# Kernel optimization log

Measured on AMD Instinct MI355X. Metric: run time of the kernel, lower is better.

## Reference

```python
import jax, jax.numpy as jnp
import numpy as np
from jax import lax

B, C_IN, N, K = 4, 128, 4096, 16
C_OUT = 256
EPS = 1e-5


def setup_inputs() -> dict:
    key = jax.random.key(0)
    k1, k2, k3, k4, k5 = jax.random.split(key, 5)
    x = jax.random.normal(k1, (B, C_IN, N, 1), dtype=jnp.float32)
    y = jax.random.normal(k2, (B, C_IN, N, 1), dtype=jnp.float32)
    edge_index = jax.random.randint(k3, (2, B, N, K), 0, N)
    # Conv2d(in=2*C_IN, out=C_OUT, kernel 3x3), kaiming-ish scale
    fan_in = 2 * C_IN * 9
    conv_w = jax.random.normal(k4, (C_OUT, 2 * C_IN, 3, 3), dtype=jnp.float32) * (2.0 / fan_in) ** 0.5
    conv_b = jnp.zeros((C_OUT,), dtype=jnp.float32)
    gamma = jnp.ones((C_OUT,), dtype=jnp.float32)
    beta = jnp.zeros((C_OUT,), dtype=jnp.float32)
    _ = k5
    return {"x": x, "y": y, "edge_index": edge_index,
            "conv_w": conv_w, "conv_b": conv_b, "gamma": gamma, "beta": beta}


def _batched_index_select(feat, idx):
    # feat: [B, C, N, 1], idx: [B, N, K] -> [B, C, N, K]
    fs = feat[..., 0]  # [B, C, N]
    return jax.vmap(lambda fb, ib: fb[:, ib])(fs, idx)


def reference(x, y, edge_index, conv_w, conv_b, gamma, beta):
    x_i = _batched_index_select(x, edge_index[1])        # [B, C, N, K]
    x_j = _batched_index_select(y, edge_index[0])        # [B, C, N, K]
    h = jnp.concatenate([x_i, x_j - x_i], axis=1)        # [B, 2C, N, K]
    out = lax.conv_general_dilated(
        h, conv_w, window_strides=(1, 1), padding=((1, 1), (1, 1)),
        dimension_numbers=("NCHW", "OIHW", "NCHW"))
    out = out + conv_b[None, :, None, None]
    # BatchNorm2d in training mode: biased batch statistics per channel
    mean = jnp.mean(out, axis=(0, 2, 3), keepdims=True)
    var = jnp.mean((out - mean) ** 2, axis=(0, 2, 3), keepdims=True)
    out = gamma[None, :, None, None] * (out - mean) * lax.rsqrt(var + EPS) + beta[None, :, None, None]
    out = jax.nn.relu(out)
    return jnp.max(out, axis=-1, keepdims=True)          # [B, C_OUT, N, 1]
```

## Files before the change

kernel.cpp:

```cpp
#include <hip/hip_runtime.h>

typedef unsigned short u16;
typedef unsigned int u32;
typedef __attribute__((ext_vector_type(8))) u16 u16x8;
typedef __attribute__((ext_vector_type(8))) __bf16 bf16x8;
typedef __attribute__((ext_vector_type(4))) float f32x4;

#define CIN 128
#define NB 4
#define NN 4096
#define KPTS 16
#define COUT 256
#define POSB 65536
#define TOTPOS 262144
#define CK 2304

__device__ __forceinline__ float bf2f(u16 u){ return __uint_as_float(((u32)u)<<16); }
__device__ __forceinline__ u16 f2bf(float f){
  u32 u = __float_as_uint(f);
  u32 r = (u + 0x7fffu + ((u>>16)&1u)) >> 16;
  return (u16)r;
}

__global__ void pack_w_kernel(const float* __restrict__ w, u16* __restrict__ wp){
  int t = blockIdx.x*256 + threadIdx.x;
  if (t >= COUT*CK) return;
  int co = t / CK; int r = t - co*CK; int tap = r >> 8; int c = r & 255;
  float v;
  if (c < 128)
    v = w[(co*256 + c)*9 + tap] - w[(co*256 + 128 + c)*9 + tap];
  else
    v = w[(co*256 + c)*9 + tap];
  wp[t] = f2bf(v);
}

__global__ void transpose_cast_kernel(const float* __restrict__ x, const float* __restrict__ y,
                                      u16* __restrict__ xt, u16* __restrict__ yt){
  __shared__ u16 tile[2][32][65];
  int n0 = blockIdx.x*64, c0 = blockIdx.y*32, b = blockIdx.z;
  int t = threadIdx.x;
  int tn = t & 63, tc = t >> 6;
  #pragma unroll
  for (int i=0;i<8;++i){
    int c = tc*8 + i;
    size_t src = ((size_t)(b*CIN + c0 + c))*NN + n0 + tn;
    tile[0][c][tn] = f2bf(x[src]);
    tile[1][c][tn] = f2bf(y[src]);
  }
  __syncthreads();
  int tcc = t & 31, tnn = t >> 5;
  #pragma unroll
  for (int i=0;i<8;++i){
    int n = tnn*8 + i;
    size_t dst = ((size_t)(b*NN + n0 + n))*CIN + c0 + tcc;
    xt[dst] = tile[0][tcc][n];
    yt[dst] = tile[1][tcc][n];
  }
}

#define SWZ(row, chunk) (((row)*32) + ((((chunk) ^ (((row)>>1)&3))) << 3))

__global__ __launch_bounds__(256) void conv_gemm_kernel(const u16* __restrict__ wp,
    const int* __restrict__ e, const u16* __restrict__ xt, const u16* __restrict__ yt,
    const u16* __restrict__ zrow, const float* __restrict__ bias,
    float* __restrict__ ssum, float* __restrict__ ssq, float* __restrict__ maxout){
  __shared__ u16 als[3*4096];
  __shared__ u16 pnl[2*6144];

  int bid = blockIdx.x;
  int co_half = (bid >> 3) & 1;
  int ptile = (bid & 7) | ((bid >> 4) << 3);
  int p0 = ptile * 128;
  int b = p0 >> 16;
  int pib0 = p0 & (POSB-1);
  int nb0 = pib0 >> 4;

  int t = threadIdx.x;
  int lane = t & 63, wave = t >> 6;
  int wr = wave >> 1, wc = wave & 1;
  int co_base = co_half*128;
  int l15 = lane & 15, l4 = lane >> 4;

  const u16* xb = xt + ((size_t)b)*NN*CIN;
  const u16* yb = yt + ((size_t)b)*NN*CIN;

  int r0 = wave*32 + (lane>>2);
  int r1 = r0 + 16;
  int ch0 = (lane&3) ^ ((r0>>1)&3);
  int ch1 = (lane&3) ^ ((r1>>1)&3);
  int wuni = __builtin_amdgcn_readfirstlane(wave);
  int wu  = wuni*1024;
  int wu2 = wuni*512;
  const u16* pA0 = wp + (size_t)(co_base + r0)*CK + ch0*8;
  const u16* pA1 = wp + (size_t)(co_base + r1)*CK + ch1*8;

  const u16 *xp[3], *yp[3];
  { int tq4 = t >> 2;
    #pragma unroll
    for (int i=0;i<3;++i){
      int row = i*64 + tq4;
      int lc = (t&3) ^ ((row>>1)&3);
      int q = (row*57) >> 10;
      int kk = row - q*18 - 1;
      int n2 = nb0 - 1 + q;
      bool valid = (row < 180) && ((unsigned)n2 < (unsigned)NN) && ((unsigned)kk < (unsigned)KPTS);
      int j0 = 0, j1 = 0;
      if (valid){ int eo = b*POSB + n2*16 + kk; j0 = e[eo]; j1 = e[TOTPOS + eo]; }
      xp[i] = (valid ? xb + (size_t)j1*CIN : zrow) + lc*8;
      yp[i] = (valid ? yb + (size_t)j0*CIN : zrow) + lc*8;
    }
  }

  auto G16 = [&](const u16* g, u16* l){
    __builtin_amdgcn_global_load_lds((const __attribute__((address_space(1))) u32*)g,
                                     (__attribute__((address_space(3))) u32*)l, 16, 0, 0);
  };

  f32x4 acc[4][4];
  #pragma unroll
  for (int i=0;i<4;++i)
    #pragma unroll
    for (int j=0;j<4;++j) acc[i][j] = (f32x4){0.f,0.f,0.f,0.f};

  G16(xp[0],    &pnl[wu2]);
  G16(xp[1],    &pnl[2048+wu2]);
  G16(xp[2],    &pnl[4096+wu2]);
  G16(xp[0]+32, &pnl[6144+wu2]);
  G16(xp[1]+32, &pnl[6144+2048+wu2]);
  G16(xp[2]+32, &pnl[6144+4096+wu2]);
  G16(pA0,      &als[wu]);      G16(pA1,      &als[wu+512]);
  G16(pA0+256,  &als[4096+wu]); G16(pA1+256,  &als[4096+wu+512]);
  G16(pA0+512,  &als[8192+wu]); G16(pA1+512,  &als[8192+wu+512]);

  int aoff[4];
  #pragma unroll
  for (int f=0; f<4; ++f) aoff[f] = SWZ(wr*64 + f*16 + l15, l4);
  int wc72l15 = wc*72 + l15;

  bf16x8 f0_a[4], f0_b[4], f1_a[4], f1_b[4];

  asm volatile("s_waitcnt vmcnt(4)" ::: "memory");
  __builtin_amdgcn_s_barrier();
  #pragma unroll
  for (int f=0; f<4; ++f) f0_a[f] = *(bf16x8*)&als[aoff[f]];
  #pragma unroll
  for (int f=0; f<4; ++f){
    int r = wc72l15 + f*18;
    f0_b[f] = *(bf16x8*)&pnl[r*32 + ((l4 ^ ((r>>1)&3))<<3)];
  }

  #define STEP(TAU, CUR, NXT) { \
    asm volatile("s_waitcnt lgkmcnt(0)" ::: "memory"); \
    __builtin_amdgcn_s_barrier(); \
    { int chs = (c + (((TAU)>=6)?1:0)) & 7; \
      int koff = ((((TAU)+3)%9)*256) + (chs<<5); \
      G16(pA0 + koff, &als[(((TAU)%3)*4096) + wu]); \
      G16(pA1 + koff, &als[(((TAU)%3)*4096) + wu + 512]); } \
    if ((TAU)==0){ int cc=(c+1)&7; int co32=(cc&3)*32; \
      const u16* s0=(cc<4?xp[0]:yp[0])+co32; \
      const u16* s1=(cc<4?xp[1]:yp[1])+co32; \
      const u16* s2=(cc<4?xp[2]:yp[2])+co32; \
      int pd=((c+1)&1)*6144; \
      G16(s0,&pnl[pd+wu2]); G16(s1,&pnl[pd+2048+wu2]); G16(s2,&pnl[pd+4096+wu2]); } \
    if ((TAU)<=1) asm volatile("s_waitcnt vmcnt(7)" ::: "memory"); \
    else          asm volatile("s_waitcnt vmcnt(4)" ::: "memory"); \
    __builtin_amdgcn_s_barrier(); \
    if ((c < 7) || ((TAU) < 8)){ \
      _Pragma("unroll") \
      for (int f=0; f<4; ++f) NXT##_a[f] = *(bf16x8*)&als[((((TAU)+1)%3)*4096) + aoff[f]]; \
      const u16* pb = ((TAU)==8) ? pbN : pbC; \
      const int tq = ((TAU)+1)%9; \
      const int kbc = (tq/3)*18 + (tq%3); \
      _Pragma("unroll") \
      for (int f=0; f<4; ++f){ int r = wc72l15 + kbc + f*18; \
        NXT##_b[f] = *(bf16x8*)&pb[r*32 + ((l4 ^ ((r>>1)&3))<<3)]; } \
    } \
    __builtin_amdgcn_sched_barrier(0); \
    __builtin_amdgcn_s_setprio(1); \
    _Pragma("unroll") \
    for (int fm=0; fm<4; ++fm) \
      _Pragma("unroll") \
      for (int fn=0; fn<4; ++fn) \
        acc[fm][fn] = __builtin_amdgcn_mfma_f32_16x16x32_bf16(CUR##_a[fm], CUR##_b[fn], acc[fm][fn], 0, 0, 0); \
    __builtin_amdgcn_s_setprio(0); \
  }

  for (int cp = 0; cp < 8; cp += 2){
    {
      int c = cp;
      const u16* pbC = pnl;
      const u16* pbN = pnl + 6144;
      STEP(0, f0, f1)  STEP(1, f1, f0)  STEP(2, f0, f1)
      STEP(3, f1, f0)  STEP(4, f0, f1)  STEP(5, f1, f0)
      STEP(6, f0, f1)  STEP(7, f1, f0)  STEP(8, f0, f1)
    }
    {
      int c = cp + 1;
      const u16* pbC = pnl + 6144;
      const u16* pbN = pnl;
      STEP(0, f1, f0)  STEP(1, f0, f1)  STEP(2, f1, f0)
      STEP(3, f0, f1)  STEP(4, f1, f0)  STEP(5, f0, f1)
      STEP(6, f1, f0)  STEP(7, f0, f1)  STEP(8, f1, f0)
    }
  }
  #undef STEP

  asm volatile("s_waitcnt vmcnt(0)" ::: "memory");
  __builtin_amdgcn_s_barrier();

  float* fs = (float*)&als[0];
  fs[t & 255] = 0.f;
  __syncthreads();

  #pragma unroll
  for (int fm=0; fm<4; ++fm){
    #pragma unroll
    for (int j=0; j<4; ++j){
      int ch = wr*64 + fm*16 + l4*4 + j;
      int co_g = co_base + ch;
      float bv2 = bias[co_g];
      float s = 0.f, q = 0.f;
      float mv[4];
      #pragma unroll
      for (int fn=0; fn<4; ++fn){
        float v = acc[fm][fn][j] + bv2;
        s += v; q += v*v; mv[fn] = v;
      }
      #pragma unroll
      for (int o=1; o<16; o<<=1){
        s += __shfl_xor(s, o, 64);
        q += __shfl_xor(q, o, 64);
        #pragma unroll
        for (int fn=0; fn<4; ++fn) mv[fn] = fmaxf(mv[fn], __shfl_xor(mv[fn], o, 64));
      }
      if (l15 == 0){
        atomicAdd(&fs[ch], s);
        atomicAdd(&fs[128 + ch], q);
        size_t rowb = ((size_t)(b*COUT + co_g)) << 12;
        #pragma unroll
        for (int fn=0; fn<4; ++fn)
          maxout[rowb + nb0 + wc*4 + fn] = mv[fn];
      }
    }
  }
  __syncthreads();
  if (t < 128)      atomicAdd(&ssum[co_base + t], fs[t]);
  else if (t < 256) atomicAdd(&ssq[co_base + t - 128], fs[t]);
}

__global__ void finalize_stats_kernel(const float* __restrict__ ssum, const float* __restrict__ ssq,
                                      const float* __restrict__ gamma, const float* __restrict__ beta,
                                      float* __restrict__ scale, float* __restrict__ shift){
  int co = threadIdx.x;
  float inv = 1.0f / (float)TOTPOS;
  float mean = ssum[co]*inv;
  float var = ssq[co]*inv - mean*mean;
  float sc = gamma[co] * rsqrtf(var + 1e-5f);
  scale[co] = sc;
  shift[co] = beta[co] - mean*sc;
}

__global__ void bn_finish_kernel(float* __restrict__ out, const float* __restrict__ scale,
                                 const float* __restrict__ shift){
  int t = blockIdx.x*256 + threadIdx.x;
  int co = (t >> 12) & 255;
  float v = out[t];
  out[t] = fmaxf(fmaf(scale[co], v, shift[co]), 0.f);
}

extern "C" void kernel_launch(void* const* d_in, const int* in_sizes, int n_in,
                              void* d_out, int out_size, void* d_ws, size_t ws_size,
                              hipStream_t stream){
  const float* x = (const float*)d_in[0];
  const float* y = (const float*)d_in[1];
  const int*   e = (const int*)d_in[2];
  const float* w = (const float*)d_in[3];
  const float* bias = (const float*)d_in[4];
  const float* gamma = (const float*)d_in[5];
  const float* beta  = (const float*)d_in[6];
  float* out = (float*)d_out;

  char* ws = (char*)d_ws;
  u16*   wp    = (u16*)(ws);
  float* ssum  = (float*)(ws + 1179648);
  float* ssq   = (float*)(ws + 1180672);
  u16*   zrow  = (u16*)(ws + 1181696);
  float* scale = (float*)(ws + 1182720);
  float* shift = (float*)(ws + 1183744);
  u16*   xt    = (u16*)(ws + 1184768);
  u16*   yt    = (u16*)(ws + 5379072);

  hipMemsetAsync(ssum, 0, 3072, stream);

  pack_w_kernel<<<2304, 256, 0, stream>>>(w, wp);
  dim3 tg(NN/64, CIN/32, NB);
  transpose_cast_kernel<<<tg, 256, 0, stream>>>(x, y, xt, yt);
  conv_gemm_kernel<<<4096, 256, 0, stream>>>(wp, e, xt, yt, zrow, bias, ssum, ssq, out);
  finalize_stats_kernel<<<1, COUT, 0, stream>>>(ssum, ssq, gamma, beta, scale, shift);
  bn_finish_kernel<<<out_size/256, 256, 0, stream>>>(out, scale, shift);
}
```

Measured before the change: 382.2 us.

## Compute all 256 output channels per block to halve gather traffic

Each block now covers the full 256 output channels for its 128-position tile instead of one half, so the gathered neighbor panels are loaded once and reused across twice as many MFMAs. The grid halves, the weight LDS ring doubles, and each wave accumulates 8x4 fragments. The register double-buffering of fragments is removed: each step now waits, loads A and B fragments, then issues MFMAs. It also sets launch_bounds occupancy to 2. This raises register and LDS pressure per block, and the pipelining across steps is lost.

Result: faster. 336.5 us (-11.9%).

```diff
diff --git a/kernel.cpp b/kernel.cpp
--- a/kernel.cpp
+++ b/kernel.cpp
@@ -60,16 +60,14 @@
 
 #define SWZ(row, chunk) (((row)*32) + ((((chunk) ^ (((row)>>1)&3))) << 3))
 
-__global__ __launch_bounds__(256) void conv_gemm_kernel(const u16* __restrict__ wp,
+__global__ __launch_bounds__(256, 2) void conv_gemm_kernel(const u16* __restrict__ wp,
     const int* __restrict__ e, const u16* __restrict__ xt, const u16* __restrict__ yt,
     const u16* __restrict__ zrow, const float* __restrict__ bias,
     float* __restrict__ ssum, float* __restrict__ ssq, float* __restrict__ maxout){
-  __shared__ u16 als[3*4096];
+  __shared__ u16 als[3*8192];
   __shared__ u16 pnl[2*6144];
 
-  int bid = blockIdx.x;
-  int co_half = (bid >> 3) & 1;
-  int ptile = (bid & 7) | ((bid >> 4) << 3);
+  int ptile = blockIdx.x;
   int p0 = ptile * 128;
   int b = p0 >> 16;
   int pib0 = p0 & (POSB-1);
@@ -78,21 +76,24 @@
   int t = threadIdx.x;
   int lane = t & 63, wave = t >> 6;
   int wr = wave >> 1, wc = wave & 1;
-  int co_base = co_half*128;
   int l15 = lane & 15, l4 = lane >> 4;
 
   const u16* xb = xt + ((size_t)b)*NN*CIN;
   const u16* yb = yt + ((size_t)b)*NN*CIN;
 
-  int r0 = wave*32 + (lane>>2);
-  int r1 = r0 + 16;
+  int rr = wave*64 + (lane>>2);
+  int r0 = rr, r1 = rr+16, r2 = rr+32, r3 = rr+48;
   int ch0 = (lane&3) ^ ((r0>>1)&3);
   int ch1 = (lane&3) ^ ((r1>>1)&3);
+  int ch2 = (lane&3) ^ ((r2>>1)&3);
+  int ch3 = (lane&3) ^ ((r3>>1)&3);
   int wuni = __builtin_amdgcn_readfirstlane(wave);
-  int wu  = wuni*1024;
+  int wu  = wuni*2048;
   int wu2 = wuni*512;
-  const u16* pA0 = wp + (size_t)(co_base + r0)*CK + ch0*8;
-  const u16* pA1 = wp + (size_t)(co_base + r1)*CK + ch1*8;
+  const u16* pA0 = wp + (size_t)r0*CK + ch0*8;
+  const u16* pA1 = wp + (size_t)r1*CK + ch1*8;
+  const u16* pA2 = wp + (size_t)r2*CK + ch2*8;
+  const u16* pA3 = wp + (size_t)r3*CK + ch3*8;
 
   const u16 *xp[3], *yp[3];
   { int tq4 = t >> 2;
@@ -111,14 +112,14 @@
     }
   }
 
-  auto G16 = [&](const u16* g, u16* l){
+  auto G16 = [&](const u16* g, const u16* l){
     __builtin_amdgcn_global_load_lds((const __attribute__((address_space(1))) u32*)g,
                                      (__attribute__((address_space(3))) u32*)l, 16, 0, 0);
   };
 
-  f32x4 acc[4][4];
-  #pragma unroll
-  for (int i=0;i<4;++i)
+  f32x4 acc[8][4];
+  #pragma unroll
+  for (int i=0;i<8;++i)
     #pragma unroll
     for (int j=0;j<4;++j) acc[i][j] = (f32x4){0.f,0.f,0.f,0.f};
 
@@ -128,80 +129,59 @@
   G16(xp[0]+32, &pnl[6144+wu2]);
   G16(xp[1]+32, &pnl[6144+2048+wu2]);
   G16(xp[2]+32, &pnl[6144+4096+wu2]);
-  G16(pA0,      &als[wu]);      G16(pA1,      &als[wu+512]);
-  G16(pA0+256,  &als[4096+wu]); G16(pA1+256,  &als[4096+wu+512]);
-  G16(pA0+512,  &als[8192+wu]); G16(pA1+512,  &als[8192+wu+512]);
-
-  int aoff[4];
-  #pragma unroll
-  for (int f=0; f<4; ++f) aoff[f] = SWZ(wr*64 + f*16 + l15, l4);
+  #pragma unroll
+  for (int s=0; s<3; ++s){
+    G16(pA0+s*256, &als[s*8192+wu]);
+    G16(pA1+s*256, &als[s*8192+wu+512]);
+    G16(pA2+s*256, &als[s*8192+wu+1024]);
+    G16(pA3+s*256, &als[s*8192+wu+1536]);
+  }
+
+  int aoff[8];
+  #pragma unroll
+  for (int f=0; f<8; ++f) aoff[f] = SWZ(wr*128 + f*16 + l15, l4);
   int wc72l15 = wc*72 + l15;
 
-  bf16x8 f0_a[4], f0_b[4], f1_a[4], f1_b[4];
-
-  asm volatile("s_waitcnt vmcnt(4)" ::: "memory");
-  __builtin_amdgcn_s_barrier();
-  #pragma unroll
-  for (int f=0; f<4; ++f) f0_a[f] = *(bf16x8*)&als[aoff[f]];
-  #pragma unroll
-  for (int f=0; f<4; ++f){
-    int r = wc72l15 + f*18;
-    f0_b[f] = *(bf16x8*)&pnl[r*32 + ((l4 ^ ((r>>1)&3))<<3)];
-  }
-
-  #define STEP(TAU, CUR, NXT) { \
+  #define STEP(TAU) { \
+    if ((TAU)==1 || (TAU)==2) asm volatile("s_waitcnt vmcnt(11)" ::: "memory"); \
+    else                      asm volatile("s_waitcnt vmcnt(8)"  ::: "memory"); \
+    __builtin_amdgcn_s_barrier(); \
+    bf16x8 af[8], bv[4]; \
+    { const int abase = ((TAU)%3)*8192; \
+      _Pragma("unroll") \
+      for (int f=0; f<8; ++f) af[f] = *(bf16x8*)&als[abase + aoff[f]]; } \
+    { const u16* pb = pnl + (c&1)*6144; \
+      const int kbc = ((TAU)/3)*18 + ((TAU)%3); \
+      _Pragma("unroll") \
+      for (int f=0; f<4; ++f){ int r = wc72l15 + kbc + f*18; \
+        bv[f] = *(bf16x8*)&pb[r*32 + ((l4 ^ ((r>>1)&3))<<3)]; } } \
     asm volatile("s_waitcnt lgkmcnt(0)" ::: "memory"); \
+    __builtin_amdgcn_sched_barrier(0); \
     __builtin_amdgcn_s_barrier(); \
-    { int chs = (c + (((TAU)>=6)?1:0)) & 7; \
-      int koff = ((((TAU)+3)%9)*256) + (chs<<5); \
-      G16(pA0 + koff, &als[(((TAU)%3)*4096) + wu]); \
-      G16(pA1 + koff, &als[(((TAU)%3)*4096) + wu + 512]); } \
     if ((TAU)==0){ int cc=(c+1)&7; int co32=(cc&3)*32; \
       const u16* s0=(cc<4?xp[0]:yp[0])+co32; \
       const u16* s1=(cc<4?xp[1]:yp[1])+co32; \
       const u16* s2=(cc<4?xp[2]:yp[2])+co32; \
       int pd=((c+1)&1)*6144; \
       G16(s0,&pnl[pd+wu2]); G16(s1,&pnl[pd+2048+wu2]); G16(s2,&pnl[pd+4096+wu2]); } \
-    if ((TAU)<=1) asm volatile("s_waitcnt vmcnt(7)" ::: "memory"); \
-    else          asm volatile("s_waitcnt vmcnt(4)" ::: "memory"); \
-    __builtin_amdgcn_s_barrier(); \
-    if ((c < 7) || ((TAU) < 8)){ \
-      _Pragma("unroll") \
-      for (int f=0; f<4; ++f) NXT##_a[f] = *(bf16x8*)&als[((((TAU)+1)%3)*4096) + aoff[f]]; \
-      const u16* pb = ((TAU)==8) ? pbN : pbC; \
-      const int tq = ((TAU)+1)%9; \
-      const int kbc = (tq/3)*18 + (tq%3); \
-      _Pragma("unroll") \
-      for (int f=0; f<4; ++f){ int r = wc72l15 + kbc + f*18; \
-        NXT##_b[f] = *(bf16x8*)&pb[r*32 + ((l4 ^ ((r>>1)&3))<<3)]; } \
-    } \
-    __builtin_amdgcn_sched_barrier(0); \
+    { const int chs = (c + (((TAU)>=6)?1:0)) & 7; \
+      const int koff = ((((TAU)+3)%9)*256) + (chs<<5); \
+      const int abase = ((TAU)%3)*8192; \
+      G16(pA0 + koff, &als[abase + wu]); \
+      G16(pA1 + koff, &als[abase + wu + 512]); \
+      G16(pA2 + koff, &als[abase + wu + 1024]); \
+      G16(pA3 + koff, &als[abase + wu + 1536]); } \
     __builtin_amdgcn_s_setprio(1); \
     _Pragma("unroll") \
-    for (int fm=0; fm<4; ++fm) \
+    for (int fm=0; fm<8; ++fm) \
       _Pragma("unroll") \
       for (int fn=0; fn<4; ++fn) \
-        acc[fm][fn] = __builtin_amdgcn_mfma_f32_16x16x32_bf16(CUR##_a[fm], CUR##_b[fn], acc[fm][fn], 0, 0, 0); \
+        acc[fm][fn] = __builtin_amdgcn_mfma_f32_16x16x32_bf16(af[fm], bv[fn], acc[fm][fn], 0, 0, 0); \
     __builtin_amdgcn_s_setprio(0); \
   }
 
-  for (int cp = 0; cp < 8; cp += 2){
-    {
-      int c = cp;
-      const u16* pbC = pnl;
-      const u16* pbN = pnl + 6144;
-      STEP(0, f0, f1)  STEP(1, f1, f0)  STEP(2, f0, f1)
-      STEP(3, f1, f0)  STEP(4, f0, f1)  STEP(5, f1, f0)
-      STEP(6, f0, f1)  STEP(7, f1, f0)  STEP(8, f0, f1)
-    }
-    {
-      int c = cp + 1;
-      const u16* pbC = pnl + 6144;
-      const u16* pbN = pnl;
-      STEP(0, f1, f0)  STEP(1, f0, f1)  STEP(2, f1, f0)
-      STEP(3, f0, f1)  STEP(4, f1, f0)  STEP(5, f0, f1)
-      STEP(6, f1, f0)  STEP(7, f0, f1)  STEP(8, f1, f0)
-    }
+  for (int c = 0; c < 8; ++c){
+    STEP(0) STEP(1) STEP(2) STEP(3) STEP(4) STEP(5) STEP(6) STEP(7) STEP(8)
   }
   #undef STEP
 
@@ -209,16 +189,15 @@
   __builtin_amdgcn_s_barrier();
 
   float* fs = (float*)&als[0];
-  fs[t & 255] = 0.f;
+  fs[t] = 0.f; fs[256 + t] = 0.f;
   __syncthreads();
 
   #pragma unroll
-  for (int fm=0; fm<4; ++fm){
+  for (int fm=0; fm<8; ++fm){
     #pragma unroll
     for (int j=0; j<4; ++j){
-      int ch = wr*64 + fm*16 + l4*4 + j;
-      int co_g = co_base + ch;
-      float bv2 = bias[co_g];
+      int ch = wr*128 + fm*16 + l4*4 + j;
+      float bv2 = bias[ch];
       float s = 0.f, q = 0.f;
       float mv[4];
       #pragma unroll
@@ -235,8 +214,8 @@
       }
       if (l15 == 0){
         atomicAdd(&fs[ch], s);
-        atomicAdd(&fs[128 + ch], q);
-        size_t rowb = ((size_t)(b*COUT + co_g)) << 12;
+        atomicAdd(&fs[256 + ch], q);
+        size_t rowb = ((size_t)(b*COUT + ch)) << 12;
         #pragma unroll
         for (int fn=0; fn<4; ++fn)
           maxout[rowb + nb0 + wc*4 + fn] = mv[fn];
@@ -244,8 +223,8 @@
     }
   }
   __syncthreads();
-  if (t < 128)      atomicAdd(&ssum[co_base + t], fs[t]);
-  else if (t < 256) atomicAdd(&ssq[co_base + t - 128], fs[t]);
+  atomicAdd(&ssum[t], fs[t]);
+  atomicAdd(&ssq[t],  fs[256 + t]);
 }
 
 __global__ void finalize_stats_kernel(const float* __restrict__ ssum, const float* __restrict__ ssq,
@@ -295,7 +274,7 @@
   pack_w_kernel<<<2304, 256, 0, stream>>>(w, wp);
   dim3 tg(NN/64, CIN/32, NB);
   transpose_cast_kernel<<<tg, 256, 0, stream>>>(x, y, xt, yt);
-  conv_gemm_kernel<<<4096, 256, 0, stream>>>(wp, e, xt, yt, zrow, bias, ssum, ssq, out);
+  conv_gemm_kernel<<<2048, 256, 0, stream>>>(wp, e, xt, yt, zrow, bias, ssum, ssq, out);
   finalize_stats_kernel<<<1, COUT, 0, stream>>>(ssum, ssq, gamma, beta, scale, shift);
   bn_finish_kernel<<<out_size/256, 256, 0, stream>>>(out, scale, shift);
 }
```
